# Kernel optimization log

Measured on AMD Instinct MI355X. Metric: run time of the kernel, lower is better.

## Reference

```python
import jax, jax.numpy as jnp
import numpy as np

L, C, H, I, E, K = 2, 1024, 16, 4096, 8, 2
B, N = 4, 640
HD = C // H
SCALE = HD ** -0.5
EPS = 1e-6


def setup_inputs() -> dict:
    key = jax.random.key(0)
    ks = jax.random.split(key, 20)
    w = lambda k, shape: jax.random.normal(k, shape, dtype=jnp.float32) * 0.02
    return {
        "hidden_states": jax.random.normal(ks[0], (B, N, C), dtype=jnp.float32),
        "attention_mask": jnp.ones((B, N), dtype=jnp.int32),
        "relative_position_bias": jax.random.normal(ks[1], (H, N, N), dtype=jnp.float32),
        "qkv_w": w(ks[2], (L, 3 * C, C)),
        "q_bias": jnp.zeros((L, C), jnp.float32),
        "v_bias": jnp.zeros((L, C), jnp.float32),
        "proj_w": w(ks[3], (L, C, C)),
        "proj_b": jnp.zeros((L, C), jnp.float32),
        "ln1_s": jnp.ones((L, C), jnp.float32),
        "ln1_b": jnp.zeros((L, C), jnp.float32),
        "ln2_s": jnp.ones((L, C), jnp.float32),
        "ln2_b": jnp.zeros((L, C), jnp.float32),
        "gamma1": 0.1 * jnp.ones((L, C), jnp.float32),
        "gamma2": 0.1 * jnp.ones((L, C), jnp.float32),
        "gate_w": w(ks[4], (L, E, C)),
        "fc1_w": w(ks[5], (L, E, I, C)),
        "fc1_b": jnp.zeros((L, E, I), jnp.float32),
        "fc2_w": w(ks[6], (L, E, C, I)),
        "fc2_b": jnp.zeros((L, E, C), jnp.float32),
    }


def layer_norm(x, s, b):
    m = jnp.mean(x, axis=-1, keepdims=True)
    v = jnp.var(x, axis=-1, keepdims=True)
    return (x - m) * jax.lax.rsqrt(v + EPS) * s + b


def attention(x, mask, rpb, qkv_w, q_b, v_b, p_w, p_b):
    Bb, Nn, Cc = x.shape
    bias = jnp.concatenate([q_b, jnp.zeros_like(v_b), v_b])
    qkv = x @ qkv_w.T + bias  # [B,N,3C]
    qkv = qkv.reshape(Bb, Nn, 3, H, HD).transpose(2, 0, 3, 1, 4)  # [3,B,H,N,hd]
    q, k, v = qkv[0] * SCALE, qkv[1], qkv[2]
    attn = jnp.einsum("bhqd,bhkd->bhqk", q, k) + rpb[None]  # fp32 scores
    attn = jnp.where(mask[:, None, None, :].astype(bool), attn, -jnp.inf)
    attn = jax.nn.softmax(attn, axis=-1)
    out = jnp.einsum("bhqk,bhkd->bhqd", attn, v)
    out = out.transpose(0, 2, 1, 3).reshape(Bb, Nn, Cc)
    return out @ p_w.T + p_b


def moe_ffn(x, gate_w, fc1_w, fc1_b, fc2_w, fc2_b):
    # top-k softmax gating with renormalized combine weights (no capacity drop)
    logits = jnp.einsum("bnc,ec->bne", x, gate_w)
    probs = jax.nn.softmax(logits, axis=-1)  # [B,N,E]
    top_v, top_i = jax.lax.top_k(probs, K)  # [B,N,K]
    gates = top_v / jnp.sum(top_v, axis=-1, keepdims=True)
    onehot = jax.nn.one_hot(top_i, E, dtype=x.dtype)  # [B,N,K,E]
    combine = jnp.einsum("bnk,bnke->bne", gates, onehot)  # sparse combine weights
    # dense-per-expert compute (reference; mathematically == routed top-k)
    h = jnp.einsum("bnc,eic->bnei", x, fc1_w) + fc1_b
    h = jax.nn.gelu(h, approximate=False)
    y = jnp.einsum("bnei,eci->bnec", h, fc2_w) + fc2_b
    out = jnp.einsum("bnec,bne->bnc", y, combine)
    # load-balancing aux loss (Switch/GShard style)
    me = jnp.mean(probs.reshape(-1, E), axis=0)
    ce = jnp.mean(onehot.reshape(-1, E), axis=0) * K
    aux = E * jnp.sum(me * ce)
    return out, aux


def reference(hidden_states, attention_mask, relative_position_bias, qkv_w, q_bias,
              v_bias, proj_w, proj_b, ln1_s, ln1_b, ln2_s, ln2_b, gamma1, gamma2,
              gate_w, fc1_w, fc1_b, fc2_w, fc2_b):
    x = hidden_states
    aux_total = jnp.float32(0.0)
    for l in range(L):
        res = x
        h = layer_norm(x, ln1_s[l], ln1_b[l])
        h = attention(h, attention_mask, relative_position_bias,
                      qkv_w[l], q_bias[l], v_bias[l], proj_w[l], proj_b[l])
        x = res + h * gamma1[l]
        res = x
        h = layer_norm(x, ln2_s[l], ln2_b[l])
        h, aux = moe_ffn(h, gate_w[l], fc1_w[l], fc1_b[l], fc2_w[l], fc2_b[l])
        aux_total = aux_total + aux
        x = res + h * gamma2[l]
    return x, aux_total
```

## Files before the change

### kernel.cpp

```cpp
#include <hip/hip_runtime.h>
#include <hip/hip_bf16.h>

#define TB 4
#define TN 640
#define TC 1024
#define TH 16
#define THD 64
#define TI 4096
#define TE 8
#define TT (TB*TN)
#define TBH (TB*TH)
#define SCALE_ 0.125f
#define NT1 32
#define NT2 48

typedef unsigned short u16;
typedef __bf16 bf16x8 __attribute__((ext_vector_type(8)));
typedef float f32x4 __attribute__((ext_vector_type(4)));

__device__ __forceinline__ float gelu_tanh(float v){
  float t = 0.7978845608f*(v + 0.044715f*v*v*v);
  float e = __expf(2.f*t);
  return 0.5f*v*(1.f + (1.f - 2.f/(e + 1.f)));
}

template<int BM,int BN,int MODE,int EPI>
__global__ __launch_bounds__(512) void gemm8(
    const u16* __restrict__ A, const u16* __restrict__ Wb, void* __restrict__ Cout,
    const float* __restrict__ bias, long biasStride,
    const int* __restrict__ tE, const int* __restrict__ tL,
    const int* __restrict__ tC, const int* __restrict__ tO,
    const int* __restrict__ etok,
    int M, int Kfull, int Kchunk, int n0, int ldc, long sW, long sCk)
{
  constexpr int FM = BM/32, FN = BN/64;
  constexpr int AI = BM/64, BI = BN/64;

  const int nwg = gridDim.x;
  int lin = blockIdx.x;
  int q = nwg >> 3, r = nwg & 7;
  int xcd = lin & 7, pos = lin >> 3;
  int swz = (xcd < r ? xcd*(q+1) : r*(q+1) + (xcd-r)*q) + pos;
  const int id0 = swz % n0, id1 = swz / n0;

  int e, loc0, cnt, off0, bx;
  if constexpr (MODE == 0){
    e = 0; loc0 = id0*BM; cnt = M; off0 = 0; bx = id1;
  } else {
    bx = id0;
    e = tE[id1]; if (e < 0) return;
    loc0 = tL[id1]; cnt = tC[id1]; off0 = tO[id1];
  }
  const int kc = blockIdx.z;
  const long kbase = (long)kc * Kchunk;

  const int tid = threadIdx.x, w = tid>>6, lane = tid&63;
  const int wm = w>>2, wn = w&3;

  __shared__ __align__(16) u16 As0[BM*64], As1[BM*64];
  __shared__ __align__(16) u16 Bs0[BN*64], Bs1[BN*64];

  const u16* Wz = Wb + (long)e*sW;

  const int c16 = (lane&7) ^ ((lane>>3)&7);
  long a_src[AI];
  #pragma unroll
  for (int j=0;j<AI;j++){
    int li = (w*AI+j)*8 + (lane>>3);
    int row;
    if constexpr (MODE == 0){
      row = loc0 + li;
    } else {
      int ll = loc0 + li; if (ll > cnt-1) ll = cnt-1;
      if constexpr (MODE == 1) row = etok[e*TT + ll];
      else                     row = off0 + ll;
    }
    a_src[j] = (long)row*Kfull + kbase + c16*8;
  }
  long b_src[BI];
  #pragma unroll
  for (int j=0;j<BI;j++){
    int rr = bx*BN + (w*BI+j)*8 + (lane>>3);
    b_src[j] = (long)rr*Kfull + kbase + c16*8;
  }

  auto STAGE = [&](u16 (&Ad)[BM*64], u16 (&Bd)[BN*64], int t){
    #pragma unroll
    for (int j=0;j<AI;j++)
      __builtin_amdgcn_global_load_lds(
        (const __attribute__((address_space(1))) void*)(A + a_src[j] + t*64),
        (__attribute__((address_space(3))) void*)(&Ad[(w*AI+j)*512]), 16, 0, 0);
    #pragma unroll
    for (int j=0;j<BI;j++)
      __builtin_amdgcn_global_load_lds(
        (const __attribute__((address_space(1))) void*)(Wz + b_src[j] + t*64),
        (__attribute__((address_space(3))) void*)(&Bd[(w*BI+j)*512]), 16, 0, 0);
  };

  f32x4 acc[FM][FN];
  #pragma unroll
  for (int m=0;m<FM;m++)
    #pragma unroll
    for (int n=0;n<FN;n++) acc[m][n] = (f32x4){0.f,0.f,0.f,0.f};

  const int lr = lane & 15;
  const int s0 = (lane>>4) ^ (lane&7);
  const int abase = lr*128 + s0*16;

  auto COMP = [&](const u16 (&As)[BM*64], const u16 (&Bs)[BN*64]){
    const char* Ab = (const char*)&As[0];
    const char* Bb = (const char*)&Bs[0];
    bf16x8 af[FM][2], bfr[FN][2];
    #pragma unroll
    for (int m=0;m<FM;m++){
      af[m][0] = *reinterpret_cast<const bf16x8*>(Ab + wm*(BM/2)*128 + m*2048 + abase);
      af[m][1] = *reinterpret_cast<const bf16x8*>(Ab + wm*(BM/2)*128 + m*2048 + (abase^64));
    }
    #pragma unroll
    for (int n=0;n<FN;n++){
      bfr[n][0] = *reinterpret_cast<const bf16x8*>(Bb + wn*(BN/4)*128 + n*2048 + abase);
      bfr[n][1] = *reinterpret_cast<const bf16x8*>(Bb + wn*(BN/4)*128 + n*2048 + (abase^64));
    }
    #pragma unroll
    for (int m=0;m<FM;m++)
      #pragma unroll
      for (int n=0;n<FN;n++){
        acc[m][n] = __builtin_amdgcn_mfma_f32_16x16x32_bf16(af[m][0], bfr[n][0], acc[m][n], 0,0,0);
        acc[m][n] = __builtin_amdgcn_mfma_f32_16x16x32_bf16(af[m][1], bfr[n][1], acc[m][n], 0,0,0);
      }
  };

  const int nt = Kchunk >> 6;
  STAGE(As0, Bs0, 0);
  __syncthreads();
  for (int t=0; t<nt; t+=2){
    if (t+1 < nt) STAGE(As1, Bs1, t+1);
    COMP(As0, Bs0);
    __syncthreads();
    if (t+1 < nt){
      if (t+2 < nt) STAGE(As0, Bs0, t+2);
      COMP(As1, Bs1);
      __syncthreads();
    }
  }

  const float* bz = (bias && kc==0) ? (bias + (long)e*biasStride) : nullptr;
  #pragma unroll
  for (int m=0;m<FM;m++){
    #pragma unroll
    for (int n=0;n<FN;n++){
      int gcol = bx*BN + wn*(BN/4) + n*16 + (lane&15);
      float bv = bz ? bz[gcol] : 0.f;
      #pragma unroll
      for (int jj=0;jj<4;jj++){
        int li = wm*(BM/2) + m*16 + (lane>>4)*4 + jj;
        int ll = loc0 + li;
        if (MODE != 0 && ll >= cnt) continue;
        float v = acc[m][n][jj] + bv;
        if constexpr (EPI == 3) v = gelu_tanh(v);
        long orow = (MODE == 0) ? (long)ll : (long)(off0 + ll);
        ((__hip_bfloat16*)Cout)[kc*sCk + orow*ldc + gcol] = __float2bfloat16(v);
      }
    }
  }
}

template<int BM,int BN,int EPI>
__global__ __launch_bounds__(256) void gemm_bt(
    const u16* __restrict__ A, const u16* __restrict__ Wb, void* __restrict__ Cout,
    const float* __restrict__ bias, const float* __restrict__ scalevec,
    int M, int Kfull, int nby, int ldc)
{
  constexpr int FM = BM/32, FN = BN/32;
  constexpr int AI = BM/32, BI = BN/32;

  const int nwg = gridDim.x;
  int lin = blockIdx.x;
  int q = nwg >> 3, r = nwg & 7;
  int xcd = lin & 7, pos = lin >> 3;
  int swz = (xcd < r ? xcd*(q+1) : r*(q+1) + (xcd-r)*q) + pos;
  const int bx = swz / nby;
  const int by = swz - bx*nby;
  if (by*BM >= M) return;

  const int tid = threadIdx.x, w = tid>>6, lane = tid&63;
  const int wm = w>>1, wn = w&1;

  __shared__ __align__(16) u16 As0[BM*64], As1[BM*64];
  __shared__ __align__(16) u16 Bs0[BN*64], Bs1[BN*64];

  const int c16 = (lane&7) ^ ((lane>>3)&7);
  long a_src[AI];
  #pragma unroll
  for (int j=0;j<AI;j++){
    int i = by*BM + (w*AI+j)*8 + (lane>>3);
    a_src[j] = (long)i*Kfull + c16*8;
  }
  long b_src[BI];
  #pragma unroll
  for (int j=0;j<BI;j++){
    int rr = bx*BN + (w*BI+j)*8 + (lane>>3);
    b_src[j] = (long)rr*Kfull + c16*8;
  }

  auto STAGE = [&](u16 (&Ad)[BM*64], u16 (&Bd)[BN*64], int t){
    #pragma unroll
    for (int j=0;j<AI;j++)
      __builtin_amdgcn_global_load_lds(
        (const __attribute__((address_space(1))) void*)(A + a_src[j] + t*64),
        (__attribute__((address_space(3))) void*)(&Ad[(w*AI+j)*512]), 16, 0, 0);
    #pragma unroll
    for (int j=0;j<BI;j++)
      __builtin_amdgcn_global_load_lds(
        (const __attribute__((address_space(1))) void*)(Wb + b_src[j] + t*64),
        (__attribute__((address_space(3))) void*)(&Bd[(w*BI+j)*512]), 16, 0, 0);
  };

  f32x4 acc[FM][FN];
  #pragma unroll
  for (int m=0;m<FM;m++)
    #pragma unroll
    for (int n=0;n<FN;n++) acc[m][n] = (f32x4){0.f,0.f,0.f,0.f};

  const int lr = lane & 15;
  const int s0 = (lane>>4) ^ (lane&7);
  const int abase = lr*128 + s0*16;

  auto COMP = [&](const u16 (&As)[BM*64], const u16 (&Bs)[BN*64]){
    const char* Ab = (const char*)&As[0];
    const char* Bb = (const char*)&Bs[0];
    bf16x8 af[FM][2], bfr[FN][2];
    #pragma unroll
    for (int m=0;m<FM;m++){
      af[m][0] = *reinterpret_cast<const bf16x8*>(Ab + wm*(BM/2)*128 + m*2048 + abase);
      af[m][1] = *reinterpret_cast<const bf16x8*>(Ab + wm*(BM/2)*128 + m*2048 + (abase^64));
    }
    #pragma unroll
    for (int n=0;n<FN;n++){
      bfr[n][0] = *reinterpret_cast<const bf16x8*>(Bb + wn*(BN/2)*128 + n*2048 + abase);
      bfr[n][1] = *reinterpret_cast<const bf16x8*>(Bb + wn*(BN/2)*128 + n*2048 + (abase^64));
    }
    #pragma unroll
    for (int m=0;m<FM;m++)
      #pragma unroll
      for (int n=0;n<FN;n++){
        acc[m][n] = __builtin_amdgcn_mfma_f32_16x16x32_bf16(af[m][0], bfr[n][0], acc[m][n], 0,0,0);
        acc[m][n] = __builtin_amdgcn_mfma_f32_16x16x32_bf16(af[m][1], bfr[n][1], acc[m][n], 0,0,0);
      }
  };

  const int nt = Kfull >> 6;
  STAGE(As0, Bs0, 0);
  __syncthreads();
  for (int t=0; t<nt; t+=2){
    if (t+1 < nt) STAGE(As1, Bs1, t+1);
    COMP(As0, Bs0);
    __syncthreads();
    if (t+1 < nt){
      if (t+2 < nt) STAGE(As0, Bs0, t+2);
      COMP(As1, Bs1);
      __syncthreads();
    }
  }

  #pragma unroll
  for (int m=0;m<FM;m++){
    #pragma unroll
    for (int n=0;n<FN;n++){
      int gcol = bx*BN + wn*(BN/2) + n*16 + (lane&15);
      float bv = bias ? bias[gcol] : 0.f;
      #pragma unroll
      for (int jj=0;jj<4;jj++){
        int i = by*BM + wm*(BM/2) + m*16 + (lane>>4)*4 + jj;
        float v = acc[m][n][jj] + bv;
        float* p = (float*)Cout + (long)i*ldc + gcol;
        *p += v * scalevec[gcol];
      }
    }
  }
}

__global__ __launch_bounds__(256) void fattn(
    const u16* __restrict__ qkv, const u16* __restrict__ vT,
    const float* __restrict__ rpb, const int* __restrict__ mask, u16* __restrict__ attn_o)
{
  const int blk = blockIdx.x;
  const int bh = blk / 5, qt = blk - bh*5;
  const int b = bh >> 4, h = bh & 15;
  const int q0 = qt * 128;
  const int tid = threadIdx.x, w = tid >> 6, lane = tid & 63;

  __shared__ __align__(16) u16 Qs[128*64];
  __shared__ __align__(16) u16 Ks0[64*64], Ks1[64*64];
  __shared__ __align__(16) u16 Vs0[64*64], Vs1[64*64];
  __shared__ __align__(16) u16 Ps[4][32*72];

  const int c16 = (lane&7) ^ ((lane>>3)&7);
  const long qkbase = (long)h*THD;
  #pragma unroll
  for (int j=0;j<4;j++){
    int row = (w*4+j)*8 + (lane>>3);
    __builtin_amdgcn_global_load_lds(
      (const __attribute__((address_space(1))) void*)(qkv + (long)(b*TN + q0 + row)*(3*TC) + qkbase + c16*8),
      (__attribute__((address_space(3))) void*)(&Qs[(w*4+j)*512]), 16, 0, 0);
  }

  auto STAGE = [&](u16 (&Kd)[64*64], u16 (&Vd)[64*64], int k0){
    #pragma unroll
    for (int j=0;j<2;j++){
      int row = (w*2+j)*8 + (lane>>3);
      __builtin_amdgcn_global_load_lds(
        (const __attribute__((address_space(1))) void*)(qkv + (long)(b*TN + k0 + row)*(3*TC) + TC + qkbase + c16*8),
        (__attribute__((address_space(3))) void*)(&Kd[(w*2+j)*512]), 16, 0, 0);
      __builtin_amdgcn_global_load_lds(
        (const __attribute__((address_space(1))) void*)(vT + ((long)bh*THD + row)*TN + k0 + c16*8),
        (__attribute__((address_space(3))) void*)(&Vd[(w*2+j)*512]), 16, 0, 0);
    }
  };

  const int s0 = (lane>>4) ^ (lane&7);
  const int lr = lane & 15;

  f32x4 acc_o[2][4];
  #pragma unroll
  for (int mq=0;mq<2;mq++)
    #pragma unroll
    for (int nd=0;nd<4;nd++) acc_o[mq][nd] = (f32x4){0.f,0.f,0.f,0.f};
  float m_r[2][4], l_r[2][4];
  #pragma unroll
  for (int mq=0;mq<2;mq++)
    #pragma unroll
    for (int jj=0;jj<4;jj++){ m_r[mq][jj] = -3e38f; l_r[mq][jj] = 0.f; }

  auto TILE = [&](const u16 (&Ks)[64*64], const u16 (&Vs)[64*64], int k0){
    const char* Qb = (const char*)&Qs[0];
    const char* Kb = (const char*)&Ks[0];
    const char* Vb = (const char*)&Vs[0];
    bf16x8 qa[2][2], kf[4][2];
    #pragma unroll
    for (int mq=0;mq<2;mq++){
      int row = w*32 + mq*16 + lr;
      qa[mq][0] = *reinterpret_cast<const bf16x8*>(Qb + row*128 + s0*16);
      qa[mq][1] = *reinterpret_cast<const bf16x8*>(Qb + row*128 + (s0*16^64));
    }
    #pragma unroll
    for (int nk=0;nk<4;nk++){
      int row = nk*16 + lr;
      kf[nk][0] = *reinterpret_cast<const bf16x8*>(Kb + row*128 + s0*16);
      kf[nk][1] = *reinterpret_cast<const bf16x8*>(Kb + row*128 + (s0*16^64));
    }
    f32x4 acc_s[2][4];
    #pragma unroll
    for (int mq=0;mq<2;mq++)
      #pragma unroll
      for (int nk=0;nk<4;nk++){
        acc_s[mq][nk] = (f32x4){0.f,0.f,0.f,0.f};
        acc_s[mq][nk] = __builtin_amdgcn_mfma_f32_16x16x32_bf16(qa[mq][0], kf[nk][0], acc_s[mq][nk], 0,0,0);
        acc_s[mq][nk] = __builtin_amdgcn_mfma_f32_16x16x32_bf16(qa[mq][1], kf[nk][1], acc_s[mq][nk], 0,0,0);
      }
    float sc[2][4];
    #pragma unroll
    for (int mq=0;mq<2;mq++){
      #pragma unroll
      for (int jj=0;jj<4;jj++){
        int qrow = q0 + w*32 + mq*16 + (lane>>4)*4 + jj;
        float s[4];
        #pragma unroll
        for (int nk=0;nk<4;nk++){
          int kg = k0 + nk*16 + lr;
          float t = acc_s[mq][nk][jj]*SCALE_ + rpb[((long)h*TN + qrow)*TN + kg];
          if (mask[b*TN + kg] == 0) t = -1e30f;
          s[nk] = t;
        }
        float mx = fmaxf(fmaxf(s[0],s[1]), fmaxf(s[2],s[3]));
        #pragma unroll
        for (int o=1;o<16;o<<=1) mx = fmaxf(mx, __shfl_xor(mx, o));
        float mnew = fmaxf(m_r[mq][jj], mx);
        float scale = __expf(m_r[mq][jj] - mnew);
        float rs = 0.f;
        #pragma unroll
        for (int nk=0;nk<4;nk++){ s[nk] = __expf(s[nk] - mnew); rs += s[nk]; }
        #pragma unroll
        for (int o=1;o<16;o<<=1) rs += __shfl_xor(rs, o);
        l_r[mq][jj] = l_r[mq][jj]*scale + rs;
        m_r[mq][jj] = mnew;
        sc[mq][jj] = scale;
        int qloc = mq*16 + (lane>>4)*4 + jj;
        #pragma unroll
        for (int nk=0;nk<4;nk++)
          Ps[w][qloc*72 + nk*16 + lr] = (u16)__bfloat16_as_ushort(__float2bfloat16(s[nk]));
      }
      f32x4 sv = (f32x4){sc[mq][0], sc[mq][1], sc[mq][2], sc[mq][3]};
      #pragma unroll
      for (int nd=0;nd<4;nd++) acc_o[mq][nd] *= sv;
    }
    const char* Pw = (const char*)&Ps[w][0];
    bf16x8 pa[2][2], vb[4][2];
    #pragma unroll
    for (int mq=0;mq<2;mq++){
      int qloc = mq*16 + lr;
      pa[mq][0] = *reinterpret_cast<const bf16x8*>(Pw + qloc*144 + (lane>>4)*16);
      pa[mq][1] = *reinterpret_cast<const bf16x8*>(Pw + qloc*144 + (lane>>4)*16 + 64);
    }
    #pragma unroll
    for (int nd=0;nd<4;nd++){
      int row = nd*16 + lr;
      vb[nd][0] = *reinterpret_cast<const bf16x8*>(Vb + row*128 + s0*16);
      vb[nd][1] = *reinterpret_cast<const bf16x8*>(Vb + row*128 + (s0*16^64));
    }
    #pragma unroll
    for (int mq=0;mq<2;mq++)
      #pragma unroll
      for (int nd=0;nd<4;nd++){
        acc_o[mq][nd] = __builtin_amdgcn_mfma_f32_16x16x32_bf16(pa[mq][0], vb[nd][0], acc_o[mq][nd], 0,0,0);
        acc_o[mq][nd] = __builtin_amdgcn_mfma_f32_16x16x32_bf16(pa[mq][1], vb[nd][1], acc_o[mq][nd], 0,0,0);
      }
  };

  STAGE(Ks0, Vs0, 0);
  __syncthreads();
  for (int t=0; t<10; t+=2){
    if (t+1 < 10) STAGE(Ks1, Vs1, (t+1)*64);
    TILE(Ks0, Vs0, t*64);
    __syncthreads();
    if (t+1 < 10){
      if (t+2 < 10) STAGE(Ks0, Vs0, (t+2)*64);
      TILE(Ks1, Vs1, (t+1)*64);
      __syncthreads();
    }
  }

  #pragma unroll
  for (int mq=0;mq<2;mq++){
    float linv[4];
    #pragma unroll
    for (int jj=0;jj<4;jj++) linv[jj] = 1.f / l_r[mq][jj];
    #pragma unroll
    for (int nd=0;nd<4;nd++){
      #pragma unroll
      for (int jj=0;jj<4;jj++){
        int qg = q0 + w*32 + mq*16 + (lane>>4)*4 + jj;
        int dg = h*THD + nd*16 + lr;
        attn_o[(long)(b*TN + qg)*TC + dg] =
          (u16)__bfloat16_as_ushort(__float2bfloat16(acc_o[mq][nd][jj]*linv[jj]));
      }
    }
  }
}

__global__ __launch_bounds__(256) void v_transpose(const u16* __restrict__ qkv,
    u16* __restrict__ vT)
{
  const int bh = blockIdx.y, b = bh>>4, h = bh&15;
  const int n0 = blockIdx.x*128;
  const int tid = threadIdx.x;
  __shared__ u16 vt[128][72];
  #pragma unroll
  for (int j=0;j<4;j++){
    int f = j*2048 + tid*8;
    int r = f>>6, d = f&63;
    *(uint4*)(&vt[r][d]) = *(const uint4*)(qkv + (long)(b*TN + n0 + r)*(3*TC) + 2*TC + h*THD + d);
  }
  __syncthreads();
  #pragma unroll
  for (int j=0;j<4;j++){
    int f = j*2048 + tid*8;
    int dr = f>>7, nc = f&127;
    union { uint4 v; u16 u[8]; } o;
    #pragma unroll
    for (int e=0;e<8;e++) o.u[e] = vt[nc+e][dr];
    *(uint4*)(vT + ((long)bh*THD + dr)*TN + n0 + nc) = o.v;
  }
}

__global__ __launch_bounds__(256) void cvt2(
    const float* __restrict__ s1, u16* __restrict__ d1, long n1,
    const float* __restrict__ s2, u16* __restrict__ d2, long n2)
{
  long i = ((long)blockIdx.x*256 + threadIdx.x)*8;
  const float* s; u16* d; long k;
  if (i < n1){ s = s1; d = d1; k = i; }
  else { k = i - n1; if (k >= n2) return; s = s2; d = d2; }
  float4 a = *(const float4*)(s+k);
  float4 b = *(const float4*)(s+k+4);
  union { __hip_bfloat162 h[4]; uint4 v; } o;
  o.h[0] = __float22bfloat162_rn(make_float2(a.x,a.y));
  o.h[1] = __float22bfloat162_rn(make_float2(a.z,a.w));
  o.h[2] = __float22bfloat162_rn(make_float2(b.x,b.y));
  o.h[3] = __float22bfloat162_rn(make_float2(b.z,b.w));
  *(uint4*)(d+k) = o.v;
}

__global__ __launch_bounds__(256) void init_x_kernel(const float* __restrict__ h,
    float* __restrict__ x, int n)
{
  int i = blockIdx.x*256 + threadIdx.x;
  if (i < n) x[i] = h[i];
  else if (i == n) x[i] = 0.f;
}

__global__ __launch_bounds__(256) void ln_kernel(const float* __restrict__ x,
    const float* __restrict__ s, const float* __restrict__ b,
    __hip_bfloat16* __restrict__ ob)
{
  int row = blockIdx.x, tid = threadIdx.x;
  const float* xr = x + (long)row*TC;
  int c = tid*4;
  float4 xv = *(const float4*)(xr + c);
  float sum = xv.x+xv.y+xv.z+xv.w;
  float sq = xv.x*xv.x+xv.y*xv.y+xv.z*xv.z+xv.w*xv.w;
  #pragma unroll
  for (int o=32;o;o>>=1){ sum += __shfl_down(sum,o); sq += __shfl_down(sq,o); }
  __shared__ float ls[8];
  if ((tid&63)==0){ ls[tid>>6] = sum; ls[4+(tid>>6)] = sq; }
  __syncthreads();
  float mean = (ls[0]+ls[1]+ls[2]+ls[3]) * (1.f/TC);
  float ex2  = (ls[4]+ls[5]+ls[6]+ls[7]) * (1.f/TC);
  float rstd = rsqrtf(ex2 - mean*mean + 1e-6f);
  float4 sv = *(const float4*)(s + c);
  float4 bv = *(const float4*)(b + c);
  float o0 = (xv.x-mean)*rstd*sv.x + bv.x;
  float o1 = (xv.y-mean)*rstd*sv.y + bv.y;
  float o2 = (xv.z-mean)*rstd*sv.z + bv.z;
  float o3 = (xv.w-mean)*rstd*sv.w + bv.w;
  __hip_bfloat16* op = ob + (long)row*TC + c;
  *reinterpret_cast<__hip_bfloat162*>(op)   = __float22bfloat162_rn(make_float2(o0,o1));
  *reinterpret_cast<__hip_bfloat162*>(op+2) = __float22bfloat162_rn(make_float2(o2,o3));
}

__global__ __launch_bounds__(256) void ln_gate_kernel(const float* __restrict__ x,
    const float* __restrict__ s, const float* __restrict__ b,
    __hip_bfloat16* __restrict__ ob, const float* __restrict__ gw,
    float* __restrict__ logits, int* __restrict__ counts, float* __restrict__ psum)
{
  int row = blockIdx.x, tid = threadIdx.x;
  if (row == 0 && tid < TE){ counts[tid] = 0; psum[tid] = 0.f; }
  const float* xr = x + (long)row*TC;
  int c = tid*4;
  float4 xv = *(const float4*)(xr + c);
  float sum = xv.x+xv.y+xv.z+xv.w;
  float sq = xv.x*xv.x+xv.y*xv.y+xv.z*xv.z+xv.w*xv.w;
  #pragma unroll
  for (int o=32;o;o>>=1){ sum += __shfl_down(sum,o); sq += __shfl_down(sq,o); }
  __shared__ float ls[8];
  if ((tid&63)==0){ ls[tid>>6] = sum; ls[4+(tid>>6)] = sq; }
  __syncthreads();
  float mean = (ls[0]+ls[1]+ls[2]+ls[3]) * (1.f/TC);
  float ex2  = (ls[4]+ls[5]+ls[6]+ls[7]) * (1.f/TC);
  float rstd = rsqrtf(ex2 - mean*mean + 1e-6f);
  float4 sv = *(const float4*)(s + c);
  float4 bv = *(const float4*)(b + c);
  float o0 = (xv.x-mean)*rstd*sv.x + bv.x;
  float o1 = (xv.y-mean)*rstd*sv.y + bv.y;
  float o2 = (xv.z-mean)*rstd*sv.z + bv.z;
  float o3 = (xv.w-mean)*rstd*sv.w + bv.w;
  __hip_bfloat16* op = ob + (long)row*TC + c;
  *reinterpret_cast<__hip_bfloat162*>(op)   = __float22bfloat162_rn(make_float2(o0,o1));
  *reinterpret_cast<__hip_bfloat162*>(op+2) = __float22bfloat162_rn(make_float2(o2,o3));
  __shared__ float gs[4];
  #pragma unroll
  for (int e=0;e<TE;e++){
    float4 wv = *(const float4*)(gw + (long)e*TC + c);
    float pr = o0*wv.x + o1*wv.y + o2*wv.z + o3*wv.w;
    #pragma unroll
    for (int o=32;o;o>>=1) pr += __shfl_down(pr,o);
    if ((tid&63)==0) gs[tid>>6] = pr;
    __syncthreads();
    if (tid==0) logits[(long)row*TE + e] = gs[0]+gs[1]+gs[2]+gs[3];
    __syncthreads();
  }
}

__global__ __launch_bounds__(256) void routing_kernel(const float* __restrict__ logits,
    int* __restrict__ counts, int* __restrict__ etok,
    int* __restrict__ tEt, int* __restrict__ tPt, float* __restrict__ tGt,
    float* __restrict__ psum)
{
  __shared__ float ps[TE];
  int tid = threadIdx.x;
  if (tid < TE) ps[tid] = 0.f;
  __syncthreads();
  int t = blockIdx.x*256 + tid;
  if (t < TT){
    float pr[TE]; float mx = -3e38f;
    #pragma unroll
    for (int e=0;e<TE;e++){ pr[e] = logits[(long)t*TE+e]; mx = fmaxf(mx, pr[e]); }
    float sum = 0.f;
    #pragma unroll
    for (int e=0;e<TE;e++){ pr[e] = __expf(pr[e]-mx); sum += pr[e]; }
    float inv = 1.f/sum;
    #pragma unroll
    for (int e=0;e<TE;e++) pr[e] *= inv;
    int i1 = 0;
    #pragma unroll
    for (int e=1;e<TE;e++) if (pr[e] > pr[i1]) i1 = e;
    int i2 = -1;
    #pragma unroll
    for (int e=0;e<TE;e++){ if (e==i1) continue; if (i2<0 || pr[e]>pr[i2]) i2=e; }
    float p1 = pr[i1], p2 = pr[i2];
    float g1 = p1/(p1+p2), g2 = p2/(p1+p2);
    int pos1 = atomicAdd(&counts[i1], 1);
    etok[i1*TT + pos1] = t;
    int pos2 = atomicAdd(&counts[i2], 1);
    etok[i2*TT + pos2] = t;
    tEt[2*t] = i1; tPt[2*t] = pos1; tGt[2*t] = g1;
    tEt[2*t+1] = i2; tPt[2*t+1] = pos2; tGt[2*t+1] = g2;
    #pragma unroll
    for (int e=0;e<TE;e++) atomicAdd(&ps[e], pr[e]);
  }
  __syncthreads();
  if (tid < TE) atomicAdd(&psum[tid], ps[tid]);
}

__global__ void build_qkv_bias(const float* __restrict__ qb, const float* __restrict__ vb,
    float* __restrict__ out)
{
  int i = blockIdx.x*256 + threadIdx.x;
  if (i >= 3*TC) return;
  float v = 0.f;
  if (i < TC) v = qb[i];
  else if (i >= 2*TC) v = vb[i-2*TC];
  out[i] = v;
}

__global__ void finalize_routing(const int* __restrict__ counts, int* __restrict__ offsets,
    const float* __restrict__ psum, float* __restrict__ aux,
    int* __restrict__ tE1, int* __restrict__ tL1, int* __restrict__ tC1, int* __restrict__ tO1,
    int* __restrict__ tE2, int* __restrict__ tL2, int* __restrict__ tC2, int* __restrict__ tO2)
{
  int off = 0; float a = 0.f; int n1 = 0, n2 = 0;
  for (int e=0;e<TE;e++){
    offsets[e] = off; int c = counts[e];
    for (int j=0;j<c;j+=256){ tE1[n1]=e; tL1[n1]=j; tC1[n1]=c; tO1[n1]=off; n1++; }
    for (int j=0;j<c;j+=128){ tE2[n2]=e; tL2[n2]=j; tC2[n2]=c; tO2[n2]=off; n2++; }
    a += (psum[e]*(1.f/TT)) * ((float)c*(1.f/TT));
    off += c;
  }
  for (;n1<NT1;n1++) tE1[n1] = -1;
  for (;n2<NT2;n2++) tE2[n2] = -1;
  aux[0] += (float)TE * a;
}

__global__ __launch_bounds__(256) void combine_ln(
    const u16* __restrict__ y, long yck, const int* __restrict__ tEt,
    const int* __restrict__ tPt, const float* __restrict__ tGt,
    const int* __restrict__ offsets, const float* __restrict__ gamma2,
    float* __restrict__ x,
    const float* __restrict__ ln_s, const float* __restrict__ ln_b,
    __hip_bfloat16* __restrict__ ln_out)
{
  int t = blockIdx.x, tid = threadIdx.x, c = tid*4;
  int e1 = tEt[2*t], e2 = tEt[2*t+1];
  long s1 = (long)(offsets[e1]+tPt[2*t])*TC + c;
  long s2 = (long)(offsets[e2]+tPt[2*t+1])*TC + c;
  float g1 = tGt[2*t], g2 = tGt[2*t+1];
  ushort4 a0 = *(const ushort4*)(y+s1);
  ushort4 a1 = *(const ushort4*)(y+yck+s1);
  ushort4 b0 = *(const ushort4*)(y+s2);
  ushort4 b1 = *(const ushort4*)(y+yck+s2);
  float4 gv = *(const float4*)(gamma2 + c);
  float* xp = x + (long)t*TC + c;
  float4 xv = *(const float4*)xp;
  auto f = [](u16 u){ union{float f;unsigned i;} v; v.i = (unsigned)u<<16; return v.f; };
  xv.x += (g1*(f(a0.x)+f(a1.x)) + g2*(f(b0.x)+f(b1.x)))*gv.x;
  xv.y += (g1*(f(a0.y)+f(a1.y)) + g2*(f(b0.y)+f(b1.y)))*gv.y;
  xv.z += (g1*(f(a0.z)+f(a1.z)) + g2*(f(b0.z)+f(b1.z)))*gv.z;
  xv.w += (g1*(f(a0.w)+f(a1.w)) + g2*(f(b0.w)+f(b1.w)))*gv.w;
  *(float4*)xp = xv;
  if (!ln_out) return;
  float sum = xv.x+xv.y+xv.z+xv.w;
  float sq = xv.x*xv.x+xv.y*xv.y+xv.z*xv.z+xv.w*xv.w;
  #pragma unroll
  for (int o=32;o;o>>=1){ sum += __shfl_down(sum,o); sq += __shfl_down(sq,o); }
  __shared__ float ls[8];
  if ((tid&63)==0){ ls[tid>>6] = sum; ls[4+(tid>>6)] = sq; }
  __syncthreads();
  float mean = (ls[0]+ls[1]+ls[2]+ls[3]) * (1.f/TC);
  float ex2  = (ls[4]+ls[5]+ls[6]+ls[7]) * (1.f/TC);
  float rstd = rsqrtf(ex2 - mean*mean + 1e-6f);
  float4 sv = *(const float4*)(ln_s + c);
  float4 bv = *(const float4*)(ln_b + c);
  float o0 = (xv.x-mean)*rstd*sv.x + bv.x;
  float o1 = (xv.y-mean)*rstd*sv.y + bv.y;
  float o2 = (xv.z-mean)*rstd*sv.z + bv.z;
  float o3 = (xv.w-mean)*rstd*sv.w + bv.w;
  __hip_bfloat16* op = ln_out + (long)t*TC + c;
  *reinterpret_cast<__hip_bfloat162*>(op)   = __float22bfloat162_rn(make_float2(o0,o1));
  *reinterpret_cast<__hip_bfloat162*>(op+2) = __float22bfloat162_rn(make_float2(o2,o3));
}

extern "C" void kernel_launch(void* const* d_in, const int* in_sizes, int n_in,
                              void* d_out, int out_size, void* d_ws, size_t ws_size,
                              hipStream_t stream) {
  (void)in_sizes; (void)n_in; (void)out_size; (void)ws_size;
  const float* hidden = (const float*)d_in[0];
  const int*   amask  = (const int*)d_in[1];
  const float* rpb    = (const float*)d_in[2];
  const float* qkv_w  = (const float*)d_in[3];
  const float* q_bias = (const float*)d_in[4];
  const float* v_bias = (const float*)d_in[5];
  const float* proj_w = (const float*)d_in[6];
  const float* proj_b = (const float*)d_in[7];
  const float* ln1_s  = (const float*)d_in[8];
  const float* ln1_b  = (const float*)d_in[9];
  const float* ln2_s  = (const float*)d_in[10];
  const float* ln2_b  = (const float*)d_in[11];
  const float* gamma1 = (const float*)d_in[12];
  const float* gamma2 = (const float*)d_in[13];
  const float* gate_w = (const float*)d_in[14];
  const float* fc1_w  = (const float*)d_in[15];
  const float* fc1_b  = (const float*)d_in[16];
  const float* fc2_w  = (const float*)d_in[17];
  const float* fc2_b  = (const float*)d_in[18];

  float* x = (float*)d_out;
  const int NXC = TT*TC;

  char* p = (char*)d_ws;
  auto alloc = [&](size_t bytes)->void* {
    void* r = (void*)p; p += (bytes + 255) & ~(size_t)255; return r;
  };
  float* qkvbias = (float*)alloc(3*TC*4);
  u16*   ln_bf   = (u16*)alloc((size_t)TT*TC*2);
  float* logits  = (float*)alloc((size_t)TT*TE*4);
  int*   counts  = (int*)alloc(TE*4);
  int*   offsets = (int*)alloc(TE*4);
  float* psum    = (float*)alloc(TE*4);
  int*   etok    = (int*)alloc((size_t)TE*TT*4);
  int*   tEt     = (int*)alloc((size_t)2*TT*4);
  int*   tPt     = (int*)alloc((size_t)2*TT*4);
  float* tGt     = (float*)alloc((size_t)2*TT*4);
  int*   tE1 = (int*)alloc(NT1*4); int* tL1 = (int*)alloc(NT1*4);
  int*   tC1 = (int*)alloc(NT1*4); int* tO1 = (int*)alloc(NT1*4);
  int*   tE2 = (int*)alloc(NT2*4); int* tL2 = (int*)alloc(NT2*4);
  int*   tC2 = (int*)alloc(NT2*4); int* tO2 = (int*)alloc(NT2*4);
  char* arena = (char*)alloc(202375168);
  u16*   qkv_bf  = (u16*)(arena + 157286400);
  u16*   vT      = (u16*)(arena + 183500800);
  u16*   attn_o  = (u16*)(arena + 188743680);
  u16*   wqkv    = (u16*)(arena + 193986560);
  u16*   wproj   = (u16*)(arena + 200278016);
  u16*   fc1b    = (u16*)(arena);
  u16*   fc2b    = (u16*)(arena + 67108864);
  u16*   h1      = (u16*)(arena + 134217728);
  u16*   yslot   = (u16*)(arena + 176160768);
  const long YCK = (long)5120*TC;

  init_x_kernel<<<(NXC+1+255)/256, 256, 0, stream>>>(hidden, x, NXC);

  for (int l=0;l<2;l++){
    if (l == 0)
      ln_kernel<<<TT, 256, 0, stream>>>(x, ln1_s, ln1_b, (__hip_bfloat16*)ln_bf);
    build_qkv_bias<<<(3*TC+255)/256, 256, 0, stream>>>(q_bias + l*TC, v_bias + l*TC, qkvbias);
    cvt2<<<(4*TC*TC)/2048, 256, 0, stream>>>(
        qkv_w + (size_t)l*3*TC*TC, wqkv, (long)3*TC*TC,
        proj_w + (size_t)l*TC*TC, wproj, (long)TC*TC);
    gemm8<128,128,0,1><<<dim3(20*24,1,1), 512, 0, stream>>>(
        ln_bf, wqkv, qkv_bf, qkvbias, 0,
        nullptr, nullptr, nullptr, nullptr, nullptr,
        TT, TC, TC, 20, 3*TC, 0, 0);
    v_transpose<<<dim3(TN/128, TBH), 256, 0, stream>>>(qkv_bf, vT);
    fattn<<<dim3(TBH*5,1,1), 256, 0, stream>>>(qkv_bf, vT, rpb, amask, attn_o);
    cvt2<<<(2*TE*TI*TC)/2048, 256, 0, stream>>>(
        fc1_w + (size_t)l*TE*TI*TC, fc1b, (long)TE*TI*TC,
        fc2_w + (size_t)l*TE*TC*TI, fc2b, (long)TE*TC*TI);
    gemm_bt<64,128,2><<<dim3(8*40,1,1), 256, 0, stream>>>(
        attn_o, wproj, x, proj_b + l*TC, gamma1 + l*TC,
        TT, TC, 40, TC);

    ln_gate_kernel<<<TT, 256, 0, stream>>>(x, ln2_s + l*TC, ln2_b + l*TC,
        (__hip_bfloat16*)ln_bf, gate_w + (size_t)l*TE*TC, logits, counts, psum);
    routing_kernel<<<(TT+255)/256, 256, 0, stream>>>(logits, counts, etok, tEt, tPt, tGt, psum);
    finalize_routing<<<1, 1, 0, stream>>>(counts, offsets, psum, x + NXC,
        tE1, tL1, tC1, tO1, tE2, tL2, tC2, tO2);
    gemm8<256,256,1,3><<<dim3(16*NT1,1,1), 512, 0, stream>>>(
        ln_bf, fc1b, h1, fc1_b + (size_t)l*TE*TI, TI,
        tE1, tL1, tC1, tO1, etok,
        0, TC, TC, 16, TI, (long)TI*TC, 0);
    gemm8<128,128,2,1><<<dim3(8*NT2,1,2), 512, 0, stream>>>(
        h1, fc2b, yslot, fc2_b + (size_t)l*TE*TC, TC,
        tE2, tL2, tC2, tO2, nullptr,
        0, TI, TI/2, 8, TC, (long)TC*TI, YCK);
    combine_ln<<<TT, 256, 0, stream>>>(yslot, YCK, tEt, tPt, tGt, offsets,
        gamma2 + l*TC, x,
        ln1_s + (l+1)*TC, ln1_b + (l+1)*TC,
        (l == 0) ? (__hip_bfloat16*)ln_bf : nullptr);
  }
}
```

Baseline: 906.9 us.

## Fuse fp32-to-bf16 weight conversion into GEMM staging and merge routing kernels

The GEMM kernel gains a mode that loads fp32 weights into registers, converts them to bf16 and writes them to LDS itself. This removes the separate conversion passes over the large expert FC1/FC2 and QKV weights, along with their bf16 round trip through memory. The relative position bias is converted to bf16 once up front, which halves attention bias reads but adds rounding error to the scores. Routing and finalize are merged into one 1024-thread block using shared-memory counters, dropping a launch and the global atomics. The cost is that fp32 weight loads now go through registers instead of direct global-to-LDS copies, which raises register pressure and traffic per tile.

```diff
diff --git a/kernel.cpp b/kernel.cpp
--- a/kernel.cpp
+++ b/kernel.cpp
@@ -23,10 +23,14 @@
   float e = __expf(2.f*t);
   return 0.5f*v*(1.f + (1.f - 2.f/(e + 1.f)));
 }
-
-template<int BM,int BN,int MODE,int EPI>
+__device__ __forceinline__ float b2f_(u16 u){
+  union{float f;unsigned i;} v; v.i = (unsigned)u<<16; return v.f;
+}
+
+template<int BM,int BN,int MODE,int EPI,bool WF32>
 __global__ __launch_bounds__(512) void gemm8(
-    const u16* __restrict__ A, const u16* __restrict__ Wb, void* __restrict__ Cout,
+    const u16* __restrict__ A, const u16* __restrict__ Wb, const float* __restrict__ Wf,
+    void* __restrict__ Cout,
     const float* __restrict__ bias, long biasStride,
     const int* __restrict__ tE, const int* __restrict__ tL,
     const int* __restrict__ tC, const int* __restrict__ tO,
@@ -60,7 +64,8 @@
   __shared__ __align__(16) u16 As0[BM*64], As1[BM*64];
   __shared__ __align__(16) u16 Bs0[BN*64], Bs1[BN*64];
 
-  const u16* Wz = Wb + (long)e*sW;
+  const u16*  Wz16 = WF32 ? nullptr : (Wb + (long)e*sW);
+  const float* Wz32 = WF32 ? (Wf + (long)e*sW) : nullptr;
 
   const int c16 = (lane&7) ^ ((lane>>3)&7);
   long a_src[AI];
@@ -84,17 +89,39 @@
     b_src[j] = (long)rr*Kfull + kbase + c16*8;
   }
 
-  auto STAGE = [&](u16 (&Ad)[BM*64], u16 (&Bd)[BN*64], int t){
+  auto STAGE_A = [&](u16 (&Ad)[BM*64], int t){
     #pragma unroll
     for (int j=0;j<AI;j++)
       __builtin_amdgcn_global_load_lds(
         (const __attribute__((address_space(1))) void*)(A + a_src[j] + t*64),
         (__attribute__((address_space(3))) void*)(&Ad[(w*AI+j)*512]), 16, 0, 0);
+  };
+  auto STAGE_B16 = [&](u16 (&Bd)[BN*64], int t){
     #pragma unroll
     for (int j=0;j<BI;j++)
       __builtin_amdgcn_global_load_lds(
-        (const __attribute__((address_space(1))) void*)(Wz + b_src[j] + t*64),
+        (const __attribute__((address_space(1))) void*)(Wz16 + b_src[j] + t*64),
         (__attribute__((address_space(3))) void*)(&Bd[(w*BI+j)*512]), 16, 0, 0);
+  };
+  f32x4 br[2*BI];
+  auto LOADB = [&](int t){
+    #pragma unroll
+    for (int j=0;j<BI;j++){
+      const float* src = Wz32 + b_src[j] + t*64;
+      br[2*j]   = *(const f32x4*)(src);
+      br[2*j+1] = *(const f32x4*)(src+4);
+    }
+  };
+  auto WRITEB = [&](u16 (&Bd)[BN*64]){
+    #pragma unroll
+    for (int j=0;j<BI;j++){
+      union { __hip_bfloat162 h[4]; uint4 v; } o;
+      o.h[0] = __float22bfloat162_rn(make_float2(br[2*j][0],  br[2*j][1]));
+      o.h[1] = __float22bfloat162_rn(make_float2(br[2*j][2],  br[2*j][3]));
+      o.h[2] = __float22bfloat162_rn(make_float2(br[2*j+1][0],br[2*j+1][1]));
+      o.h[3] = __float22bfloat162_rn(make_float2(br[2*j+1][2],br[2*j+1][3]));
+      *(uint4*)(&Bd[(w*BI+j)*512 + lane*8]) = o.v;
+    }
   };
 
   f32x4 acc[FM][FN];
@@ -131,16 +158,33 @@
   };
 
   const int nt = Kchunk >> 6;
-  STAGE(As0, Bs0, 0);
+  if constexpr (WF32){
+    LOADB(0); STAGE_A(As0, 0); WRITEB(Bs0);
+  } else {
+    STAGE_A(As0, 0); STAGE_B16(Bs0, 0);
+  }
   __syncthreads();
   for (int t=0; t<nt; t+=2){
-    if (t+1 < nt) STAGE(As1, Bs1, t+1);
-    COMP(As0, Bs0);
-    __syncthreads();
-    if (t+1 < nt){
-      if (t+2 < nt) STAGE(As0, Bs0, t+2);
-      COMP(As1, Bs1);
+    if constexpr (WF32){
+      if (t+1 < nt){ LOADB(t+1); STAGE_A(As1, t+1); }
+      COMP(As0, Bs0);
+      if (t+1 < nt) WRITEB(Bs1);
       __syncthreads();
+      if (t+1 < nt){
+        if (t+2 < nt){ LOADB(t+2); STAGE_A(As0, t+2); }
+        COMP(As1, Bs1);
+        if (t+2 < nt) WRITEB(Bs0);
+        __syncthreads();
+      }
+    } else {
+      if (t+1 < nt){ STAGE_A(As1, t+1); STAGE_B16(Bs1, t+1); }
+      COMP(As0, Bs0);
+      __syncthreads();
+      if (t+1 < nt){
+        if (t+2 < nt){ STAGE_A(As0, t+2); STAGE_B16(Bs0, t+2); }
+        COMP(As1, Bs1);
+        __syncthreads();
+      }
     }
   }
 
@@ -282,7 +326,7 @@
 
 __global__ __launch_bounds__(256) void fattn(
     const u16* __restrict__ qkv, const u16* __restrict__ vT,
-    const float* __restrict__ rpb, const int* __restrict__ mask, u16* __restrict__ attn_o)
+    const u16* __restrict__ rpb16, const int* __restrict__ mask, u16* __restrict__ attn_o)
 {
   const int blk = blockIdx.x;
   const int bh = blk / 5, qt = blk - bh*5;
@@ -368,7 +412,7 @@
         #pragma unroll
         for (int nk=0;nk<4;nk++){
           int kg = k0 + nk*16 + lr;
-          float t = acc_s[mq][nk][jj]*SCALE_ + rpb[((long)h*TN + qrow)*TN + kg];
+          float t = acc_s[mq][nk][jj]*SCALE_ + b2f_(rpb16[((long)h*TN + qrow)*TN + kg]);
           if (mask[b*TN + kg] == 0) t = -1e30f;
           s[nk] = t;
         }
@@ -473,22 +517,19 @@
   }
 }
 
-__global__ __launch_bounds__(256) void cvt2(
-    const float* __restrict__ s1, u16* __restrict__ d1, long n1,
-    const float* __restrict__ s2, u16* __restrict__ d2, long n2)
+__global__ __launch_bounds__(256) void cvt_kernel(const float* __restrict__ s,
+    u16* __restrict__ d, long n)
 {
   long i = ((long)blockIdx.x*256 + threadIdx.x)*8;
-  const float* s; u16* d; long k;
-  if (i < n1){ s = s1; d = d1; k = i; }
-  else { k = i - n1; if (k >= n2) return; s = s2; d = d2; }
-  float4 a = *(const float4*)(s+k);
-  float4 b = *(const float4*)(s+k+4);
+  if (i >= n) return;
+  float4 a = *(const float4*)(s+i);
+  float4 b = *(const float4*)(s+i+4);
   union { __hip_bfloat162 h[4]; uint4 v; } o;
   o.h[0] = __float22bfloat162_rn(make_float2(a.x,a.y));
   o.h[1] = __float22bfloat162_rn(make_float2(a.z,a.w));
   o.h[2] = __float22bfloat162_rn(make_float2(b.x,b.y));
   o.h[3] = __float22bfloat162_rn(make_float2(b.z,b.w));
-  *(uint4*)(d+k) = o.v;
+  *(uint4*)(d+i) = o.v;
 }
 
 __global__ __launch_bounds__(256) void init_x_kernel(const float* __restrict__ h,
@@ -531,10 +572,9 @@
 __global__ __launch_bounds__(256) void ln_gate_kernel(const float* __restrict__ x,
     const float* __restrict__ s, const float* __restrict__ b,
     __hip_bfloat16* __restrict__ ob, const float* __restrict__ gw,
-    float* __restrict__ logits, int* __restrict__ counts, float* __restrict__ psum)
+    float* __restrict__ logits)
 {
   int row = blockIdx.x, tid = threadIdx.x;
-  if (row == 0 && tid < TE){ counts[tid] = 0; psum[tid] = 0.f; }
   const float* xr = x + (long)row*TC;
   int c = tid*4;
   float4 xv = *(const float4*)(xr + c);
@@ -571,17 +611,18 @@
   }
 }
 
-__global__ __launch_bounds__(256) void routing_kernel(const float* __restrict__ logits,
-    int* __restrict__ counts, int* __restrict__ etok,
-    int* __restrict__ tEt, int* __restrict__ tPt, float* __restrict__ tGt,
-    float* __restrict__ psum)
-{
+__global__ __launch_bounds__(1024) void routing_fin(const float* __restrict__ logits,
+    int* __restrict__ etok, int* __restrict__ tEt, int* __restrict__ tPt,
+    float* __restrict__ tGt, int* __restrict__ offsets, float* __restrict__ aux,
+    int* __restrict__ tE1, int* __restrict__ tL1, int* __restrict__ tC1, int* __restrict__ tO1,
+    int* __restrict__ tE2, int* __restrict__ tL2, int* __restrict__ tC2, int* __restrict__ tO2)
+{
+  __shared__ int cnt[TE];
   __shared__ float ps[TE];
   int tid = threadIdx.x;
-  if (tid < TE) ps[tid] = 0.f;
+  if (tid < TE){ cnt[tid] = 0; ps[tid] = 0.f; }
   __syncthreads();
-  int t = blockIdx.x*256 + tid;
-  if (t < TT){
+  for (int t = tid; t < TT; t += 1024){
     float pr[TE]; float mx = -3e38f;
     #pragma unroll
     for (int e=0;e<TE;e++){ pr[e] = logits[(long)t*TE+e]; mx = fmaxf(mx, pr[e]); }
@@ -599,9 +640,9 @@
     for (int e=0;e<TE;e++){ if (e==i1) continue; if (i2<0 || pr[e]>pr[i2]) i2=e; }
     float p1 = pr[i1], p2 = pr[i2];
     float g1 = p1/(p1+p2), g2 = p2/(p1+p2);
-    int pos1 = atomicAdd(&counts[i1], 1);
+    int pos1 = atomicAdd(&cnt[i1], 1);
     etok[i1*TT + pos1] = t;
-    int pos2 = atomicAdd(&counts[i2], 1);
+    int pos2 = atomicAdd(&cnt[i2], 1);
     etok[i2*TT + pos2] = t;
     tEt[2*t] = i1; tPt[2*t] = pos1; tGt[2*t] = g1;
     tEt[2*t+1] = i2; tPt[2*t+1] = pos2; tGt[2*t+1] = g2;
@@ -609,7 +650,19 @@
     for (int e=0;e<TE;e++) atomicAdd(&ps[e], pr[e]);
   }
   __syncthreads();
-  if (tid < TE) atomicAdd(&psum[tid], ps[tid]);
+  if (tid == 0){
+    int off = 0; float a = 0.f; int n1 = 0, n2 = 0;
+    for (int e=0;e<TE;e++){
+      offsets[e] = off; int c = cnt[e];
+      for (int j=0;j<c;j+=256){ tE1[n1]=e; tL1[n1]=j; tC1[n1]=c; tO1[n1]=off; n1++; }
+      for (int j=0;j<c;j+=128){ tE2[n2]=e; tL2[n2]=j; tC2[n2]=c; tO2[n2]=off; n2++; }
+      a += (ps[e]*(1.f/TT)) * ((float)c*(1.f/TT));
+      off += c;
+    }
+    for (;n1<NT1;n1++) tE1[n1] = -1;
+    for (;n2<NT2;n2++) tE2[n2] = -1;
+    aux[0] += (float)TE * a;
+  }
 }
 
 __global__ void build_qkv_bias(const float* __restrict__ qb, const float* __restrict__ vb,
@@ -621,24 +674,6 @@
   if (i < TC) v = qb[i];
   else if (i >= 2*TC) v = vb[i-2*TC];
   out[i] = v;
-}
-
-__global__ void finalize_routing(const int* __restrict__ counts, int* __restrict__ offsets,
-    const float* __restrict__ psum, float* __restrict__ aux,
-    int* __restrict__ tE1, int* __restrict__ tL1, int* __restrict__ tC1, int* __restrict__ tO1,
-    int* __restrict__ tE2, int* __restrict__ tL2, int* __restrict__ tC2, int* __restrict__ tO2)
-{
-  int off = 0; float a = 0.f; int n1 = 0, n2 = 0;
-  for (int e=0;e<TE;e++){
-    offsets[e] = off; int c = counts[e];
-    for (int j=0;j<c;j+=256){ tE1[n1]=e; tL1[n1]=j; tC1[n1]=c; tO1[n1]=off; n1++; }
-    for (int j=0;j<c;j+=128){ tE2[n2]=e; tL2[n2]=j; tC2[n2]=c; tO2[n2]=off; n2++; }
-    a += (psum[e]*(1.f/TT)) * ((float)c*(1.f/TT));
-    off += c;
-  }
-  for (;n1<NT1;n1++) tE1[n1] = -1;
-  for (;n2<NT2;n2++) tE2[n2] = -1;
-  aux[0] += (float)TE * a;
 }
 
 __global__ __launch_bounds__(256) void combine_ln(
@@ -661,11 +696,10 @@
   float4 gv = *(const float4*)(gamma2 + c);
   float* xp = x + (long)t*TC + c;
   float4 xv = *(const float4*)xp;
-  auto f = [](u16 u){ union{float f;unsigned i;} v; v.i = (unsigned)u<<16; return v.f; };
-  xv.x += (g1*(f(a0.x)+f(a1.x)) + g2*(f(b0.x)+f(b1.x)))*gv.x;
-  xv.y += (g1*(f(a0.y)+f(a1.y)) + g2*(f(b0.y)+f(b1.y)))*gv.y;
-  xv.z += (g1*(f(a0.z)+f(a1.z)) + g2*(f(b0.z)+f(b1.z)))*gv.z;
-  xv.w += (g1*(f(a0.w)+f(a1.w)) + g2*(f(b0.w)+f(b1.w)))*gv.w;
+  xv.x += (g1*(b2f_(a0.x)+b2f_(a1.x)) + g2*(b2f_(b0.x)+b2f_(b1.x)))*gv.x;
+  xv.y += (g1*(b2f_(a0.y)+b2f_(a1.y)) + g2*(b2f_(b0.y)+b2f_(b1.y)))*gv.y;
+  xv.z += (g1*(b2f_(a0.z)+b2f_(a1.z)) + g2*(b2f_(b0.z)+b2f_(b1.z)))*gv.z;
+  xv.w += (g1*(b2f_(a0.w)+b2f_(a1.w)) + g2*(b2f_(b0.w)+b2f_(b1.w)))*gv.w;
   *(float4*)xp = xv;
   if (!ln_out) return;
   float sum = xv.x+xv.y+xv.z+xv.w;
@@ -723,9 +757,7 @@
   float* qkvbias = (float*)alloc(3*TC*4);
   u16*   ln_bf   = (u16*)alloc((size_t)TT*TC*2);
   float* logits  = (float*)alloc((size_t)TT*TE*4);
-  int*   counts  = (int*)alloc(TE*4);
   int*   offsets = (int*)alloc(TE*4);
-  float* psum    = (float*)alloc(TE*4);
   int*   etok    = (int*)alloc((size_t)TE*TT*4);
   int*   tEt     = (int*)alloc((size_t)2*TT*4);
   int*   tPt     = (int*)alloc((size_t)2*TT*4);
@@ -734,51 +766,44 @@
   int*   tC1 = (int*)alloc(NT1*4); int* tO1 = (int*)alloc(NT1*4);
   int*   tE2 = (int*)alloc(NT2*4); int* tL2 = (int*)alloc(NT2*4);
   int*   tC2 = (int*)alloc(NT2*4); int* tO2 = (int*)alloc(NT2*4);
+  u16*   rpb16   = (u16*)alloc((size_t)TH*TN*TN*2);
   char* arena = (char*)alloc(202375168);
   u16*   qkv_bf  = (u16*)(arena + 157286400);
   u16*   vT      = (u16*)(arena + 183500800);
   u16*   attn_o  = (u16*)(arena + 188743680);
-  u16*   wqkv    = (u16*)(arena + 193986560);
   u16*   wproj   = (u16*)(arena + 200278016);
-  u16*   fc1b    = (u16*)(arena);
-  u16*   fc2b    = (u16*)(arena + 67108864);
-  u16*   h1      = (u16*)(arena + 134217728);
-  u16*   yslot   = (u16*)(arena + 176160768);
+  u16*   h1      = (u16*)(arena);
+  u16*   yslot   = (u16*)(arena + 41943040);
   const long YCK = (long)5120*TC;
 
   init_x_kernel<<<(NXC+1+255)/256, 256, 0, stream>>>(hidden, x, NXC);
+  cvt_kernel<<<(TH*TN*TN)/2048, 256, 0, stream>>>(rpb, rpb16, (long)TH*TN*TN);
 
   for (int l=0;l<2;l++){
     if (l == 0)
       ln_kernel<<<TT, 256, 0, stream>>>(x, ln1_s, ln1_b, (__hip_bfloat16*)ln_bf);
     build_qkv_bias<<<(3*TC+255)/256, 256, 0, stream>>>(q_bias + l*TC, v_bias + l*TC, qkvbias);
-    cvt2<<<(4*TC*TC)/2048, 256, 0, stream>>>(
-        qkv_w + (size_t)l*3*TC*TC, wqkv, (long)3*TC*TC,
-        proj_w + (size_t)l*TC*TC, wproj, (long)TC*TC);
-    gemm8<128,128,0,1><<<dim3(20*24,1,1), 512, 0, stream>>>(
-        ln_bf, wqkv, qkv_bf, qkvbias, 0,
+    cvt_kernel<<<(TC*TC)/2048, 256, 0, stream>>>(proj_w + (size_t)l*TC*TC, wproj, (long)TC*TC);
+    gemm8<128,128,0,1,true><<<dim3(20*24,1,1), 512, 0, stream>>>(
+        ln_bf, nullptr, qkv_w + (size_t)l*3*TC*TC, qkv_bf, qkvbias, 0,
         nullptr, nullptr, nullptr, nullptr, nullptr,
         TT, TC, TC, 20, 3*TC, 0, 0);
     v_transpose<<<dim3(TN/128, TBH), 256, 0, stream>>>(qkv_bf, vT);
-    fattn<<<dim3(TBH*5,1,1), 256, 0, stream>>>(qkv_bf, vT, rpb, amask, attn_o);
-    cvt2<<<(2*TE*TI*TC)/2048, 256, 0, stream>>>(
-        fc1_w + (size_t)l*TE*TI*TC, fc1b, (long)TE*TI*TC,
-        fc2_w + (size_t)l*TE*TC*TI, fc2b, (long)TE*TC*TI);
+    fattn<<<dim3(TBH*5,1,1), 256, 0, stream>>>(qkv_bf, vT, rpb16, amask, attn_o);
     gemm_bt<64,128,2><<<dim3(8*40,1,1), 256, 0, stream>>>(
         attn_o, wproj, x, proj_b + l*TC, gamma1 + l*TC,
         TT, TC, 40, TC);
 
     ln_gate_kernel<<<TT, 256, 0, stream>>>(x, ln2_s + l*TC, ln2_b + l*TC,
-        (__hip_bfloat16*)ln_bf, gate_w + (size_t)l*TE*TC, logits, counts, psum);
-    routing_kernel<<<(TT+255)/256, 256, 0, stream>>>(logits, counts, etok, tEt, tPt, tGt, psum);
-    finalize_routing<<<1, 1, 0, stream>>>(counts, offsets, psum, x + NXC,
+        (__hip_bfloat16*)ln_bf, gate_w + (size_t)l*TE*TC, logits);
+    routing_fin<<<1, 1024, 0, stream>>>(logits, etok, tEt, tPt, tGt, offsets, x + NXC,
         tE1, tL1, tC1, tO1, tE2, tL2, tC2, tO2);
-    gemm8<256,256,1,3><<<dim3(16*NT1,1,1), 512, 0, stream>>>(
-        ln_bf, fc1b, h1, fc1_b + (size_t)l*TE*TI, TI,
+    gemm8<256,256,1,3,true><<<dim3(16*NT1,1,1), 512, 0, stream>>>(
+        ln_bf, nullptr, fc1_w + (size_t)l*TE*TI*TC, h1, fc1_b + (size_t)l*TE*TI, TI,
         tE1, tL1, tC1, tO1, etok,
         0, TC, TC, 16, TI, (long)TI*TC, 0);
-    gemm8<128,128,2,1><<<dim3(8*NT2,1,2), 512, 0, stream>>>(
-        h1, fc2b, yslot, fc2_b + (size_t)l*TE*TC, TC,
+    gemm8<128,128,2,1,true><<<dim3(8*NT2,1,2), 512, 0, stream>>>(
+        h1, nullptr, fc2_w + (size_t)l*TE*TC*TI, yslot, fc2_b + (size_t)l*TE*TC, TC,
         tE2, tL2, tC2, tO2, nullptr,
         0, TI, TI/2, 8, TC, (long)TC*TI, YCK);
     combine_ln<<<TT, 256, 0, stream>>>(yslot, YCK, tEt, tPt, tGt, offsets,
```

Measured after the change: 998.5 us. +10.1%, slower.
